# Kernel tuning notes

Hardware: AMD Instinct MI355X
Metric: run time of the kernel (lower is better)

Reference implementation:

```python
import jax, jax.numpy as jnp
import numpy as np

MIN_NEAR = 0.05
DENSITY_SCALE = 1.0
BOUND = 1.0  # spherical scene bounds radius
GEO = 15


def _density_mlp(x, dW1, db1, dW2, db2, dW3, db3):
    h = jax.nn.relu(x @ dW1 + db1)
    h = jax.nn.relu(h @ dW2 + db2)
    h = h @ dW3 + db3  # [M, 1+GEO]
    sigma = jnp.exp(jnp.clip(h[..., 0], -15.0, 15.0))  # trunc_exp
    return sigma, h[..., 1:]


def _color_mlp(d, geo, cW1, cb1, cW2, cb2, cW3, cb3):
    h = jnp.concatenate([d, geo], axis=-1)
    h = jax.nn.relu(h @ cW1 + cb1)
    h = jax.nn.relu(h @ cW2 + cb2)
    return jax.nn.sigmoid(h @ cW3 + cb3)


def _comp_weights(deltas, sigmas):
    # alpha compositing: w_i = alpha_i * prod_{j<i}(1 - alpha_j)
    alphas = 1.0 - jnp.exp(-deltas * sigmas)
    trans = jnp.cumprod(
        jnp.concatenate([jnp.ones_like(alphas[:, :1]), 1.0 - alphas + 1e-15], axis=-1),
        axis=-1)[:, :-1]
    return alphas * trans


def _sample_pdf(bins, weights, n_samples):
    # deterministic importance resampling (eval mode); bins [N,T-1], weights [N,T-2]
    weights = weights + 1e-5
    pdf = weights / jnp.sum(weights, axis=-1, keepdims=True)
    cdf = jnp.cumsum(pdf, axis=-1)
    cdf = jnp.concatenate([jnp.zeros_like(cdf[:, :1]), cdf], axis=-1)  # [N, T-1]
    u = jnp.linspace(0.5 / n_samples, 1.0 - 0.5 / n_samples, n_samples)
    u = jnp.broadcast_to(u, (bins.shape[0], n_samples))
    inds = jax.vmap(lambda c, uu: jnp.searchsorted(c, uu, side='right'))(cdf, u)
    below = jnp.clip(inds - 1, 0, cdf.shape[-1] - 1)
    above = jnp.clip(inds, 0, cdf.shape[-1] - 1)
    cdf_g0 = jnp.take_along_axis(cdf, below, axis=-1)
    cdf_g1 = jnp.take_along_axis(cdf, above, axis=-1)
    bmax = bins.shape[-1] - 1
    bins_g0 = jnp.take_along_axis(bins, jnp.clip(below, 0, bmax), axis=-1)
    bins_g1 = jnp.take_along_axis(bins, jnp.clip(above, 0, bmax), axis=-1)
    denom = jnp.where(cdf_g1 - cdf_g0 < 1e-5, 1.0, cdf_g1 - cdf_g0)
    t = (u - cdf_g0) / denom
    return bins_g0 + t * (bins_g1 - bins_g0)


def _run(rays_o, rays_d, dW1, db1, dW2, db2, dW3, db3,
         cW1, cb1, cW2, cb2, cW3, cb3, num_steps, upsample_steps):
    N = rays_o.shape[0]
    # get_z_val_bounds: ray/sphere intersection, sphere radius BOUND at origin
    b = jnp.sum(rays_o * rays_d, axis=-1)
    c = jnp.sum(rays_o * rays_o, axis=-1) - BOUND ** 2
    disc = jnp.maximum(b * b - c, 0.0)
    z_max = jnp.maximum(-b + jnp.sqrt(disc), MIN_NEAR + 1e-3)
    z_min = jnp.full_like(z_max, MIN_NEAR)
    # get_foreground_z_vals: per-ray linspace (perturb=False)
    t = jnp.linspace(0.0, 1.0, num_steps)
    z_vals = z_min[:, None] + (z_max - z_min)[:, None] * t[None, :]
    z_vals = jnp.clip(z_vals, z_min[:, None], z_max[:, None])
    xyzs = rays_o[:, None, :] + rays_d[:, None, :] * z_vals[..., None]
    sigma, geo = _density_mlp(xyzs.reshape(-1, 3), dW1, db1, dW2, db2, dW3, db3)
    sigma = sigma.reshape(N, num_steps)
    geo = geo.reshape(N, num_steps, GEO)

    # upsample_z_values: importance resampling from coarse weights
    deltas = z_vals[:, 1:] - z_vals[:, :-1]
    aug = jnp.concatenate([deltas, deltas[:, -1:]], axis=-1)
    w_coarse = _comp_weights(aug, DENSITY_SCALE * sigma)
    z_mid = 0.5 * (z_vals[:, :-1] + z_vals[:, 1:])
    new_z = jax.lax.stop_gradient(_sample_pdf(z_mid, w_coarse[:, 1:-1], upsample_steps))
    new_xyzs = rays_o[:, None, :] + rays_d[:, None, :] * new_z[..., None]
    new_sigma, new_geo = _density_mlp(new_xyzs.reshape(-1, 3), dW1, db1, dW2, db2, dW3, db3)
    new_sigma = new_sigma.reshape(N, upsample_steps)
    new_geo = new_geo.reshape(N, upsample_steps, GEO)

    # sort/gather merge of coarse + fine samples
    z_all = jnp.concatenate([z_vals, new_z], axis=1)
    order = jnp.argsort(z_all, axis=1)
    z_vals = jnp.take_along_axis(z_all, order, axis=1)  # [N, T]
    xyzs = jnp.take_along_axis(jnp.concatenate([xyzs, new_xyzs], axis=1), order[..., None], axis=1)
    sigma = jnp.take_along_axis(jnp.concatenate([sigma, new_sigma], axis=1), order, axis=1)
    geo = jnp.take_along_axis(jnp.concatenate([geo, new_geo], axis=1), order[..., None], axis=1)

    deltas = z_vals[:, 1:] - z_vals[:, :-1]
    aug = jnp.concatenate([deltas, deltas[:, -1:]], axis=-1)
    weights = _comp_weights(aug, DENSITY_SCALE * sigma)  # [N, T]

    mask = weights > 1e-4
    dirs = jnp.broadcast_to(rays_d[:, None, :], xyzs.shape).reshape(-1, 3)
    rgb = _color_mlp(dirs, geo.reshape(-1, GEO), cW1, cb1, cW2, cb2, cW3, cb3)
    rgbs = jnp.where(mask.reshape(-1, 1), rgb, 0.0).reshape(N, -1, 3)

    weights_sum = jnp.sum(weights, axis=-1)
    depth = jnp.sum(weights * z_vals, axis=-1)
    image = jnp.sum(weights[..., None] * rgbs, axis=-2)
    bg = 206.0 / 255.0
    image = image + (1.0 - weights_sum)[..., None] * bg

    # pairwise distortion loss (the (z_shifted - z_shifted) term in the source is identically zero)
    sample_dist = 1.0 / num_steps
    z_shift = jnp.concatenate([z_vals[:, 1:], jnp.full((N, 1), sample_dist, z_vals.dtype)], axis=-1)
    mid_zs = 0.5 * z_vals + 0.5 * z_shift
    pair = jnp.abs(mid_zs[:, None, :] - mid_zs[:, :, None]) * (weights[:, None, :] * weights[:, :, None])
    loss = jnp.sum(pair, axis=(1, 2)) / (depth + 1e-6)
    loss = jnp.where(loss < 1e-3, 0.0, loss)  # cutoff
    return jnp.concatenate([image, depth[:, None], loss[:, None]], axis=-1)  # [N, 5]


def setup_inputs() -> dict:
    key = jax.random.key(0)
    ks = jax.random.split(key, 16)
    N, H = 2048, 256
    rays_o = 0.1 * jax.random.normal(ks[0], (N, 3), jnp.float32)  # near scene centre
    rd = jax.random.normal(ks[1], (N, 3), jnp.float32)
    rays_d = rd / jnp.linalg.norm(rd, axis=-1, keepdims=True)

    def w(k, shape):
        return jax.random.normal(k, shape, jnp.float32) * (1.0 / np.sqrt(shape[0]))

    return {
        'rays_o': rays_o, 'rays_d': rays_d,
        'dW1': w(ks[2], (3, H)), 'db1': jnp.zeros(H, jnp.float32),
        'dW2': w(ks[3], (H, H)), 'db2': jnp.zeros(H, jnp.float32),
        'dW3': w(ks[4], (H, 1 + GEO)), 'db3': jnp.zeros(1 + GEO, jnp.float32),
        'cW1': w(ks[5], (3 + GEO, H)), 'cb1': jnp.zeros(H, jnp.float32),
        'cW2': w(ks[6], (H, H)), 'cb2': jnp.zeros(H, jnp.float32),
        'cW3': w(ks[7], (H, 3)), 'cb3': jnp.zeros(3, jnp.float32),
        'num_steps': 128, 'upsample_steps': 128,
    }


def reference(rays_o, rays_d, dW1, db1, dW2, db2, dW3, db3,
              cW1, cb1, cW2, cb2, cW3, cb3, num_steps, upsample_steps):
    return _run(rays_o, rays_d, dW1, db1, dW2, db2, dW3, db3,
                cW1, cb1, cW2, cb2, cW3, cb3, num_steps, upsample_steps)
```

## Files before the change

kernel.cpp:

```cpp
#include <hip/hip_runtime.h>


typedef float f32x4 __attribute__((ext_vector_type(4)));
typedef __bf16 bf16x8 __attribute__((ext_vector_type(8)));
typedef __bf16 bf16x4 __attribute__((ext_vector_type(4)));
typedef unsigned short u16x8 __attribute__((ext_vector_type(8)));
typedef unsigned short u16x4 __attribute__((ext_vector_type(4)));

#define NRAYS 2048
#define NSTEP 128
#define MIN_NEAR 0.05f

#define OFF_D1 0
#define OFF_D2 8192
#define OFF_D3 73728
#define OFF_C1 77824
#define OFF_C2 86016
#define OFF_C3 151552
#define PACK_TOTAL 155648

__device__ __forceinline__ unsigned short f2bf(float f) {
  __bf16 h = (__bf16)f;
  return __builtin_bit_cast(unsigned short, h);
}
__device__ __forceinline__ u16x4 pack4(float a, float b, float c, float d) {
  bf16x4 h;
  h[0] = (__bf16)a; h[1] = (__bf16)b; h[2] = (__bf16)c; h[3] = (__bf16)d;
  return __builtin_bit_cast(u16x4, h);
}

__device__ __forceinline__ float ray_z(const float* __restrict__ ro,
                                       const float* __restrict__ rd, int r, int i) {
  float ox = ro[r * 3], oy = ro[r * 3 + 1], oz = ro[r * 3 + 2];
  float dx = rd[r * 3], dy = rd[r * 3 + 1], dz = rd[r * 3 + 2];
  float b = ox * dx + oy * dy + oz * dz;
  float c = ox * ox + oy * oy + oz * oz - 1.0f;
  float disc = fmaxf(b * b - c, 0.0f);
  float zmax = fmaxf(-b + sqrtf(disc), MIN_NEAR + 1e-3f);
  float zmin = MIN_NEAR;
  float tt = (float)i / 127.0f;
  float zz = zmin + (zmax - zmin) * tt;
  return fminf(fmaxf(zz, zmin), zmax);
}

__device__ __forceinline__ float wave_iscan(float v, int lane) {
#pragma unroll
  for (int off = 1; off < 64; off <<= 1) {
    float y = __shfl_up(v, off, 64);
    if (lane >= off) v += y;
  }
  return v;
}
__device__ __forceinline__ float block_iscan(float v, float* part, int lane, int wid) {
  float s = wave_iscan(v, lane);
  if (lane == 63) part[wid] = s;
  __syncthreads();
  float pre = 0.f;
  if (wid > 0) pre += part[0];
  if (wid > 1) pre += part[1];
  if (wid > 2) pre += part[2];
  return s + pre;
}

__device__ __forceinline__ void pack_std(const float* __restrict__ W,
                                         unsigned short* __restrict__ dst,
                                         int idx, int K, int Norig, int NT) {
  int per = NT * 512;
  int kt = idx / per, rm = idx % per;
  int nt = rm >> 9, lane = (rm >> 3) & 63, j = rm & 7;
  int k = kt * 32 + ((lane >> 4) << 3) + j;
  int n = nt * 16 + (lane & 15);
  float v = (k < K && n < Norig) ? W[k * Norig + n] : 0.0f;
  dst[idx] = f2bf(v);
}

__global__ void k_pack_all(const float* __restrict__ dW1, const float* __restrict__ dW2,
                           const float* __restrict__ dW3, const float* __restrict__ cW1,
                           const float* __restrict__ cW2, const float* __restrict__ cW3,
                           unsigned short* __restrict__ Wp) {
  int idx = blockIdx.x * 256 + threadIdx.x;
  if (idx < OFF_D2) {
    pack_std(dW1, Wp + OFF_D1, idx - OFF_D1, 3, 256, 16);
  } else if (idx < OFF_D3) {
    pack_std(dW2, Wp + OFF_D2, idx - OFF_D2, 256, 256, 16);
  } else if (idx < OFF_C1) {
    int j2 = idx - OFF_D3;
    int lane = (j2 >> 3) & 63, jj = j2 & 7, kt = j2 >> 9;
    int k = kt * 32 + ((lane >> 4) << 3) + jj;
    int n = lane & 15;
    Wp[idx] = f2bf(dW3[k * 16 + ((n + 1) & 15)]);
  } else if (idx < OFF_C2) {
    int j2 = idx - OFF_C1;
    int nt = j2 >> 9, lane = (j2 >> 3) & 63, jj = j2 & 7;
    int k = ((lane >> 4) << 3) + jj;
    int n = nt * 16 + (lane & 15);
    float v = 0.0f;
    if (k < 15) v = cW1[(3 + k) * 256 + n];
    else if (k >= 16 && k < 19) v = cW1[(k - 16) * 256 + n];
    Wp[idx] = f2bf(v);
  } else if (idx < OFF_C3) {
    pack_std(cW2, Wp + OFF_C2, idx - OFF_C2, 256, 256, 16);
  } else if (idx < PACK_TOTAL) {
    pack_std(cW3, Wp + OFF_C3, idx - OFF_C3, 256, 3, 1);
  }
}


__device__ __forceinline__ void mlp_l1(const unsigned short* xb, unsigned short* buf,
                                       const bf16x8 (&w1r)[4], const float* sb1,
                                       int wid, int quad, int col) {
#pragma unroll
  for (int h = 0; h < 2; ++h) {
    f32x4 acc[8];
#pragma unroll
    for (int i = 0; i < 8; ++i) acc[i] = (f32x4){0.f, 0.f, 0.f, 0.f};
    int p0 = (h * 2) * 16 + col, p1 = (h * 2 + 1) * 16 + col;
    bf16x8 x0 = *reinterpret_cast<const bf16x8*>(&xb[p0 * 32 + ((quad ^ (p0 & 3)) * 8)]);
    bf16x8 x1 = *reinterpret_cast<const bf16x8*>(&xb[p1 * 32 + ((quad ^ (p1 & 3)) * 8)]);
#pragma unroll
    for (int ntl = 0; ntl < 4; ++ntl) {
      acc[ntl * 2 + 0] = __builtin_amdgcn_mfma_f32_16x16x32_bf16(w1r[ntl], x0, acc[ntl * 2 + 0], 0, 0, 0);
      acc[ntl * 2 + 1] = __builtin_amdgcn_mfma_f32_16x16x32_bf16(w1r[ntl], x1, acc[ntl * 2 + 1], 0, 0, 0);
    }
#pragma unroll
    for (int ntl = 0; ntl < 4; ++ntl) {
      int n = (wid * 4 + ntl) * 16 + quad * 4;
      f32x4 bv = *reinterpret_cast<const f32x4*>(&sb1[n]);
#pragma unroll
      for (int j = 0; j < 2; ++j) {
        int p = (h * 2 + j) * 16 + col;
        *reinterpret_cast<u16x4*>(&buf[p * 256 + (((n >> 3) ^ (p & 31)) * 8) + (n & 7)]) =
            pack4(fmaxf(acc[ntl * 2 + j][0] + bv[0], 0.f), fmaxf(acc[ntl * 2 + j][1] + bv[1], 0.f),
                  fmaxf(acc[ntl * 2 + j][2] + bv[2], 0.f), fmaxf(acc[ntl * 2 + j][3] + bv[3], 0.f));
      }
    }
  }
}

__device__ __forceinline__ void l2_half_compute(const unsigned short* buf,
                                                const bf16x8 (&w2r)[8][4],
                                                f32x4 (&acc)[8], int h, int quad, int col) {
#pragma unroll
  for (int i = 0; i < 8; ++i) acc[i] = (f32x4){0.f, 0.f, 0.f, 0.f};
#pragma unroll
  for (int kt = 0; kt < 8; ++kt) {
    int p0 = (h * 2) * 16 + col, p1 = (h * 2 + 1) * 16 + col;
    bf16x8 x0 = *reinterpret_cast<const bf16x8*>(&buf[p0 * 256 + (((kt * 4 + quad) ^ (p0 & 31)) * 8)]);
    bf16x8 x1 = *reinterpret_cast<const bf16x8*>(&buf[p1 * 256 + (((kt * 4 + quad) ^ (p1 & 31)) * 8)]);
#pragma unroll
    for (int ntl = 0; ntl < 4; ++ntl) {
      acc[ntl * 2 + 0] = __builtin_amdgcn_mfma_f32_16x16x32_bf16(w2r[kt][ntl], x0, acc[ntl * 2 + 0], 0, 0, 0);
      acc[ntl * 2 + 1] = __builtin_amdgcn_mfma_f32_16x16x32_bf16(w2r[kt][ntl], x1, acc[ntl * 2 + 1], 0, 0, 0);
    }
  }
}

__device__ __forceinline__ void l2_half_write(unsigned short* buf, const f32x4 (&acc)[8],
                                              const float* sb2, int h, int wid, int quad, int col) {
#pragma unroll
  for (int ntl = 0; ntl < 4; ++ntl) {
    int n = (wid * 4 + ntl) * 16 + quad * 4;
    f32x4 bv = *reinterpret_cast<const f32x4*>(&sb2[n]);
#pragma unroll
    for (int j = 0; j < 2; ++j) {
      int p = (h * 2 + j) * 16 + col;
      *reinterpret_cast<u16x4*>(&buf[p * 256 + (((n >> 3) ^ (p & 31)) * 8) + (n & 7)]) =
          pack4(fmaxf(acc[ntl * 2 + j][0] + bv[0], 0.f), fmaxf(acc[ntl * 2 + j][1] + bv[1], 0.f),
                fmaxf(acc[ntl * 2 + j][2] + bv[2], 0.f), fmaxf(acc[ntl * 2 + j][3] + bv[3], 0.f));
    }
  }
}

template <bool FIRST>
__global__ __launch_bounds__(256, 2)
void k_density(const float* __restrict__ ro, const float* __restrict__ rd,
               const float* __restrict__ zin,
               const unsigned short* __restrict__ Wp1, const float* __restrict__ b1,
               const unsigned short* __restrict__ Wp2, const float* __restrict__ b2,
               const unsigned short* __restrict__ Wp3, const float* __restrict__ b3,
               unsigned short* __restrict__ gout, float* __restrict__ sig,
               float* __restrict__ z_f) {
  __shared__ __align__(16) unsigned short buf[64 * 256];
  __shared__ __align__(16) unsigned short xb[64 * 32];
  __shared__ __align__(16) unsigned short sW3[4096];
  __shared__ __align__(16) float sb1[256];
  __shared__ __align__(16) float sb2[256];
  __shared__ __align__(16) float sb3[16];
  __shared__ __align__(16) float ssig[256];
  __shared__ __align__(16) float sred[16];
  const int t = threadIdx.x;
  const int lane = t & 63, wid = t >> 6, quad = lane >> 4, col = lane & 15;
  const int p_ = t >> 2, g_ = t & 3;

  sb1[t] = b1[t];
  sb2[t] = b2[t];
  if (t < 16) sb3[t] = b3[(t + 1) & 15];
  { const u16x8* s = (const u16x8*)Wp3; u16x8* d = (u16x8*)sW3;
    d[t] = s[t]; d[t + 256] = s[t + 256]; }

  bf16x8 w1r[4], w2r[8][4];
#pragma unroll
  for (int ntl = 0; ntl < 4; ++ntl)
    w1r[ntl] = *reinterpret_cast<const bf16x8*>(Wp1 + ((wid * 4 + ntl) * 64 + lane) * 8);
#pragma unroll
  for (int kt = 0; kt < 8; ++kt)
#pragma unroll
    for (int ntl = 0; ntl < 4; ++ntl)
      w2r[kt][ntl] = *reinterpret_cast<const bf16x8*>(Wp2 + ((kt * 16 + wid * 4 + ntl) * 64 + lane) * 8);

#pragma unroll 1
  for (int tt = 0; tt < 4; ++tt) {
    const int P0 = blockIdx.x * 256 + tt * 64;
    {
      u16x8 pk = {0, 0, 0, 0, 0, 0, 0, 0};
      if (g_ == 0) {
        int P = P0 + p_;
        int rr_ = P >> 7, ii = P & 127;
        float zz;
        if constexpr (FIRST) zz = ray_z(ro, rd, rr_, ii);
        else zz = zin[P];
        pk[0] = f2bf(ro[rr_ * 3 + 0] + rd[rr_ * 3 + 0] * zz);
        pk[1] = f2bf(ro[rr_ * 3 + 1] + rd[rr_ * 3 + 1] * zz);
        pk[2] = f2bf(ro[rr_ * 3 + 2] + rd[rr_ * 3 + 2] * zz);
      }
      *reinterpret_cast<u16x8*>(&xb[p_ * 32 + ((g_ ^ (p_ & 3)) * 8)]) = pk;
    }
    __syncthreads();
    mlp_l1(xb, buf, w1r, sb1, wid, quad, col);
    __syncthreads();
    f32x4 acc[8];
    l2_half_compute(buf, w2r, acc, 0, quad, col);
    __syncthreads();
    l2_half_write(buf, acc, sb2, 0, wid, quad, col);
    l2_half_compute(buf, w2r, acc, 1, quad, col);
    __syncthreads();
    l2_half_write(buf, acc, sb2, 1, wid, quad, col);
    __syncthreads();
    {
      const int p = wid * 16 + col;
      f32x4 a3 = {0.f, 0.f, 0.f, 0.f};
#pragma unroll
      for (int kt = 0; kt < 8; ++kt) {
        bf16x8 w = *reinterpret_cast<const bf16x8*>(&sW3[(kt * 64 + lane) * 8]);
        bf16x8 xx = *reinterpret_cast<const bf16x8*>(&buf[p * 256 + (((kt * 4 + quad) ^ (p & 31)) * 8)]);
        a3 = __builtin_amdgcn_mfma_f32_16x16x32_bf16(w, xx, a3, 0, 0, 0);
      }
      int n0 = quad * 4;
      float v0 = a3[0] + sb3[n0], v1 = a3[1] + sb3[n0 + 1];
      float v2 = a3[2] + sb3[n0 + 2], v3 = a3[3] + sb3[n0 + 3];
      if (quad == 3) {
        float sgm = __expf(fminf(fmaxf(v3, -15.f), 15.f));
        sig[P0 + p] = sgm;
        if constexpr (FIRST) ssig[tt * 64 + p] = sgm;
        v3 = 0.0f;
      }
      *reinterpret_cast<u16x4*>(gout + (size_t)(P0 + p) * 16 + n0) = pack4(v0, v1, v2, v3);
    }
  }

  if constexpr (FIRST) {
    __syncthreads();
    float* psz = reinterpret_cast<float*>(buf);
    float* pmid = psz + 256;
    float* pcdf = psz + 512;
    float* psw = psz + 768;
    const int segw = t >> 7;
    const int i = t & 127;
    const int seg = segw * 128;
    const int rg = blockIdx.x * 2 + segw;
    float zi = ray_z(ro, rd, rg, i);
    psz[seg + i] = zi;
    float sgv = ssig[t];
    __syncthreads();
    float aug = (i < 127) ? psz[seg + i + 1] - zi : psz[seg + 127] - psz[seg + 126];
    float alpha = 1.0f - __expf(-aug * sgv);
    float lt = __logf(1.0f - alpha + 1e-15f);
    float s = wave_iscan(lt, lane);
    if (lane == 63) sred[wid] = s;
    __syncthreads();
    if (wid & 1) s += sred[wid - 1];
    float w = alpha * __expf(s - lt);
    psw[seg + i] = w;
    if (i < 127) pmid[seg + i] = 0.5f * (zi + psz[seg + i + 1]);
    __syncthreads();
    float v2s = (i < 126) ? psw[seg + i + 1] + 1e-5f : 0.f;
    float s2 = wave_iscan(v2s, lane);
    if (lane == 63) sred[8 + wid] = s2;
    __syncthreads();
    if (wid & 1) s2 += sred[8 + wid - 1];
    psw[seg + i] = s2;
    __syncthreads();
    float total = psw[seg + 125];
    if (i <= 126) pcdf[seg + i] = (i == 0) ? 0.f : psw[seg + i - 1] / total;
    __syncthreads();
    const float lo = 0.5f / 128.0f, hi = 1.0f - 0.5f / 128.0f;
    float u = lo + (hi - lo) * ((float)i / 127.0f);
    int loI = 0, hiI = 127;
    while (loI < hiI) {
      int mid = (loI + hiI) >> 1;
      if (pcdf[seg + mid] > u) hiI = mid; else loI = mid + 1;
    }
    int below = loI - 1; if (below < 0) below = 0; if (below > 126) below = 126;
    int above = loI;     if (above > 126) above = 126;
    float c0 = pcdf[seg + below], c1 = pcdf[seg + above];
    float b0v = pmid[seg + below], b1v = pmid[seg + above];
    float dn = c1 - c0; if (dn < 1e-5f) dn = 1.0f;
    float ttt = (u - c0) / dn;
    z_f[rg * NSTEP + i] = b0v + ttt * (b1v - b0v);
  }
}

__global__ __launch_bounds__(256, 2)
void k_mcf(const float* __restrict__ ro, const float* __restrict__ rd,
           const float* __restrict__ z_f,
           const float* __restrict__ sigc, const float* __restrict__ sigf,
           const unsigned short* __restrict__ goutc, const unsigned short* __restrict__ goutf,
           const unsigned short* __restrict__ Wp1, const float* __restrict__ cb1,
           const unsigned short* __restrict__ Wp2, const float* __restrict__ cb2,
           const unsigned short* __restrict__ Wp3, const float* __restrict__ cb3,
           float* __restrict__ out) {
  __shared__ __align__(16) unsigned short buf[64 * 256];
  __shared__ __align__(16) unsigned short xb[64 * 32];
  __shared__ __align__(16) unsigned short sW3[4096];
  __shared__ __align__(16) float sb1[256];
  __shared__ __align__(16) float sb2[256];
  __shared__ __align__(16) float szm[256];
  __shared__ __align__(16) float swgt[256];
  __shared__ __align__(16) float srgb[768];
  __shared__ __align__(16) float sred[48];
  __shared__ unsigned short sord[256];
  const int t = threadIdx.x;
  const int lane = t & 63, wid = t >> 6, quad = lane >> 4, col = lane & 15;
  const int p_ = t >> 2, g_ = t & 3;
  const int r = blockIdx.x;

  sb1[t] = cb1[t];
  sb2[t] = cb2[t];
  { const u16x8* s = (const u16x8*)Wp3; u16x8* d = (u16x8*)sW3;
    d[t] = s[t]; d[t + 256] = s[t + 256]; }

  bf16x8 w1r[4], w2r[8][4];
#pragma unroll
  for (int ntl = 0; ntl < 4; ++ntl)
    w1r[ntl] = *reinterpret_cast<const bf16x8*>(Wp1 + ((wid * 4 + ntl) * 64 + lane) * 8);
#pragma unroll
  for (int kt = 0; kt < 8; ++kt)
#pragma unroll
    for (int ntl = 0; ntl < 4; ++ntl)
      w2r[kt][ntl] = *reinterpret_cast<const bf16x8*>(Wp2 + ((kt * 16 + wid * 4 + ntl) * 64 + lane) * 8);

  float* szc = reinterpret_cast<float*>(buf);
  float* szf = szc + 128;
  if (t < 128) szc[t] = ray_z(ro, rd, r, t);
  else szf[t - 128] = z_f[r * NSTEP + (t - 128)];
  __syncthreads();
  int pos; float myz;
  if (t < 128) {
    myz = szc[t];
    int lo = 0, hi = 128;
    while (lo < hi) { int m = (lo + hi) >> 1; if (szf[m] < myz) lo = m + 1; else hi = m; }
    pos = t + lo;
  } else {
    int j = t - 128; myz = szf[j];
    int lo = 0, hi = 128;
    while (lo < hi) { int m = (lo + hi) >> 1; if (szc[m] <= myz) lo = m + 1; else hi = m; }
    pos = j + lo;
  }
  szm[pos] = myz; sord[pos] = (unsigned short)t;
  __syncthreads();
  int srci = sord[t];
  float sg = (srci < 128) ? sigc[r * NSTEP + srci] : sigf[r * NSTEP + (srci - 128)];
  float zt = szm[t];
  float aug = (t < 255) ? szm[t + 1] - zt : szm[255] - szm[254];
  float alpha = 1.0f - __expf(-aug * sg);
  float lt = __logf(1.0f - alpha + 1e-15f);
  float incl = block_iscan(lt, sred, lane, wid);
  swgt[t] = alpha * __expf(incl - lt);
  __syncthreads();

  float dv0 = rd[r * 3], dv1 = rd[r * 3 + 1], dv2 = rd[r * 3 + 2];
  u16x8 dirpk = {f2bf(dv0), f2bf(dv1), f2bf(dv2), 0, 0, 0, 0, 0};
  u16x8 gx = {0, 0, 0, 0, 0, 0, 0, 0};
  float wgtv = 0.0f;
  {
    if (g_ < 2) {
      int s0 = sord[p_];
      const unsigned short* gs = ((s0 < 128) ? goutc : goutf)
          + ((size_t)(r * NSTEP + (s0 & 127)) * 16) + g_ * 8;
      gx = *reinterpret_cast<const u16x8*>(gs);
    } else if (g_ == 2) {
      gx = dirpk;
    } else {
      wgtv = swgt[p_];
    }
  }
#pragma unroll 1
  for (int tt = 0; tt < 4; ++tt) {
    const int haveNext = (tt < 3);
    int go = __syncthreads_or((g_ == 3) && (wgtv > 1e-4f));
    int ordn = 0; float wgtn = 0.0f;
    u16x8 gxn = {0, 0, 0, 0, 0, 0, 0, 0};
    if (go) {
      *reinterpret_cast<u16x8*>(&xb[p_ * 32 + ((g_ ^ (p_ & 3)) * 8)]) = gx;
      __syncthreads();
      mlp_l1(xb, buf, w1r, sb1, wid, quad, col);
      __syncthreads();
    }
    if (haveNext) {
      int Pn = (tt + 1) * 64 + p_;
      if (g_ < 2) ordn = sord[Pn];
      else if (g_ == 2) gxn = dirpk;
      else wgtn = swgt[Pn];
    }
    f32x4 acc[8];
    if (go) {
      l2_half_compute(buf, w2r, acc, 0, quad, col);
      __syncthreads();
      l2_half_write(buf, acc, sb2, 0, wid, quad, col);
    }
    if (haveNext && g_ < 2) {
      const unsigned short* gs = ((ordn < 128) ? goutc : goutf)
          + ((size_t)(r * NSTEP + (ordn & 127)) * 16) + g_ * 8;
      gxn = *reinterpret_cast<const u16x8*>(gs);
    }
    if (go) {
      l2_half_compute(buf, w2r, acc, 1, quad, col);
      __syncthreads();
      l2_half_write(buf, acc, sb2, 1, wid, quad, col);
      __syncthreads();
      {
        const int p = wid * 16 + col;
        f32x4 a3 = {0.f, 0.f, 0.f, 0.f};
#pragma unroll
        for (int kt = 0; kt < 8; ++kt) {
          bf16x8 w = *reinterpret_cast<const bf16x8*>(&sW3[(kt * 64 + lane) * 8]);
          bf16x8 xx = *reinterpret_cast<const bf16x8*>(&buf[p * 256 + (((kt * 4 + quad) ^ (p & 31)) * 8)]);
          a3 = __builtin_amdgcn_mfma_f32_16x16x32_bf16(w, xx, a3, 0, 0, 0);
        }
        if (quad == 0) {
          int pi = tt * 64 + p;
          srgb[pi * 3 + 0] = 1.0f / (1.0f + __expf(-(a3[0] + cb3[0])));
          srgb[pi * 3 + 1] = 1.0f / (1.0f + __expf(-(a3[1] + cb3[1])));
          srgb[pi * 3 + 2] = 1.0f / (1.0f + __expf(-(a3[2] + cb3[2])));
        }
      }
    }
    gx = gxn; wgtv = wgtn;
  }

  __syncthreads();
  float ztf = szm[t], wtf = swgt[t];
  float znext = (t < 255) ? szm[t + 1] : (1.0f / 128.0f);
  float mt = 0.5f * ztf + 0.5f * znext;
  float cr = 0.f, cg = 0.f, cbl = 0.f;
  if (wtf > 1e-4f) { cr = srgb[t * 3]; cg = srgb[t * 3 + 1]; cbl = srgb[t * 3 + 2]; }
  if (t == 255) { sred[36] = mt; sred[37] = wtf; }
  float wm = (t < 255) ? wtf : 0.f;
  float Pw = block_iscan(wm, sred, lane, wid);
  float Ps = block_iscan(wm * mt, sred + 4, lane, wid);
  float W254 = sred[0] + sred[1] + sred[2] + sred[3];
  float S254 = sred[4] + sred[5] + sred[6] + sred[7];
  float m255 = sred[36], w255 = sred[37];
  float contrib = 0.f;
  if (t < 255)
    contrib = wtf * (mt * (2.f * Pw - W254) - (2.f * Ps - S254))
            + 2.f * wtf * fabsf(mt - m255) * w255;
  float vals[6] = {wtf, wtf * ztf, wtf * cr, wtf * cg, wtf * cbl, contrib};
#pragma unroll
  for (int k = 0; k < 6; ++k) {
    float v = vals[k];
#pragma unroll
    for (int m = 1; m < 64; m <<= 1) v += __shfl_xor(v, m, 64);
    if (lane == 0) sred[8 + k * 4 + wid] = v;
  }
  __syncthreads();
  if (t == 0) {
    float a6[6];
#pragma unroll
    for (int k = 0; k < 6; ++k)
      a6[k] = sred[8 + k * 4] + sred[8 + k * 4 + 1] + sred[8 + k * 4 + 2] + sred[8 + k * 4 + 3];
    const float bgc = 206.0f / 255.0f;
    float wsum = a6[0], depth = a6[1];
    float loss = a6[5] / (depth + 1e-6f);
    if (loss < 1e-3f) loss = 0.0f;
    out[r * 5 + 0] = a6[2] + (1.0f - wsum) * bgc;
    out[r * 5 + 1] = a6[3] + (1.0f - wsum) * bgc;
    out[r * 5 + 2] = a6[4] + (1.0f - wsum) * bgc;
    out[r * 5 + 3] = depth;
    out[r * 5 + 4] = loss;
  }
}

extern "C" void kernel_launch(void* const* d_in, const int* in_sizes, int n_in,
                              void* d_out, int out_size, void* d_ws, size_t ws_size,
                              hipStream_t stream) {
  const float* rays_o = (const float*)d_in[0];
  const float* rays_d = (const float*)d_in[1];
  const float* dW1 = (const float*)d_in[2];
  const float* db1 = (const float*)d_in[3];
  const float* dW2 = (const float*)d_in[4];
  const float* db2 = (const float*)d_in[5];
  const float* dW3 = (const float*)d_in[6];
  const float* db3 = (const float*)d_in[7];
  const float* cW1 = (const float*)d_in[8];
  const float* cb1 = (const float*)d_in[9];
  const float* cW2 = (const float*)d_in[10];
  const float* cb2 = (const float*)d_in[11];
  const float* cW3 = (const float*)d_in[12];
  const float* cb3 = (const float*)d_in[13];

  char* ws = (char*)d_ws;
  size_t off = 0;
  auto alloc = [&](size_t bytes) -> void* {
    void* p = ws + off;
    off += (bytes + 255) & ~(size_t)255;
    return p;
  };
  unsigned short* Wp = (unsigned short*)alloc((size_t)PACK_TOTAL * 2);
  unsigned short* goutc = (unsigned short*)alloc((size_t)NRAYS * NSTEP * 16 * 2);
  unsigned short* goutf = (unsigned short*)alloc((size_t)NRAYS * NSTEP * 16 * 2);
  float* sigc = (float*)alloc((size_t)NRAYS * NSTEP * 4);
  float* sigf = (float*)alloc((size_t)NRAYS * NSTEP * 4);
  float* z_f  = (float*)alloc((size_t)NRAYS * NSTEP * 4);
  (void)ws_size; (void)in_sizes; (void)n_in; (void)out_size;

  k_pack_all<<<PACK_TOTAL / 256, 256, 0, stream>>>(dW1, dW2, dW3, cW1, cW2, cW3, Wp);

  k_density<true><<<(NRAYS * NSTEP) / 256, 256, 0, stream>>>(
      rays_o, rays_d, nullptr,
      Wp + OFF_D1, db1, Wp + OFF_D2, db2, Wp + OFF_D3, db3, goutc, sigc, z_f);
  k_density<false><<<(NRAYS * NSTEP) / 256, 256, 0, stream>>>(
      rays_o, rays_d, z_f,
      Wp + OFF_D1, db1, Wp + OFF_D2, db2, Wp + OFF_D3, db3, goutf, sigf, nullptr);
  k_mcf<<<NRAYS, 256, 0, stream>>>(
      rays_o, rays_d, z_f, sigc, sigf, goutc, goutf,
      Wp + OFF_C1, cb1, Wp + OFF_C2, cb2, Wp + OFF_C3, cb3, (float*)d_out);
}
```

Before: 272.2 us.

## Cut register pressure to fit three blocks per CU in MLP kernels

Restructures the layer-2 MFMA loop to process one 16-point quarter at a time (4 accumulators instead of 8), reloads layer-1 weights from global inside mlp_l1 instead of keeping them resident, and drops the software prefetch of the next tile's gathered features in the color kernel. The aim is to lower VGPR usage enough to raise launch bounds from 2 to 3 blocks per CU, improving latency hiding. The cost is more block barriers per tile (four instead of two in layer 2), repeated layer-1 weight loads, and the loss of load/compute overlap from the removed prefetch.

```diff
diff --git a/kernel.cpp b/kernel.cpp
--- a/kernel.cpp
+++ b/kernel.cpp
@@ -106,73 +106,57 @@
 }
 
 
-__device__ __forceinline__ void mlp_l1(const unsigned short* xb, unsigned short* buf,
-                                       const bf16x8 (&w1r)[4], const float* sb1,
-                                       int wid, int quad, int col) {
-#pragma unroll
-  for (int h = 0; h < 2; ++h) {
-    f32x4 acc[8];
-#pragma unroll
-    for (int i = 0; i < 8; ++i) acc[i] = (f32x4){0.f, 0.f, 0.f, 0.f};
-    int p0 = (h * 2) * 16 + col, p1 = (h * 2 + 1) * 16 + col;
-    bf16x8 x0 = *reinterpret_cast<const bf16x8*>(&xb[p0 * 32 + ((quad ^ (p0 & 3)) * 8)]);
-    bf16x8 x1 = *reinterpret_cast<const bf16x8*>(&xb[p1 * 32 + ((quad ^ (p1 & 3)) * 8)]);
-#pragma unroll
-    for (int ntl = 0; ntl < 4; ++ntl) {
-      acc[ntl * 2 + 0] = __builtin_amdgcn_mfma_f32_16x16x32_bf16(w1r[ntl], x0, acc[ntl * 2 + 0], 0, 0, 0);
-      acc[ntl * 2 + 1] = __builtin_amdgcn_mfma_f32_16x16x32_bf16(w1r[ntl], x1, acc[ntl * 2 + 1], 0, 0, 0);
-    }
-#pragma unroll
-    for (int ntl = 0; ntl < 4; ++ntl) {
-      int n = (wid * 4 + ntl) * 16 + quad * 4;
-      f32x4 bv = *reinterpret_cast<const f32x4*>(&sb1[n]);
-#pragma unroll
-      for (int j = 0; j < 2; ++j) {
-        int p = (h * 2 + j) * 16 + col;
-        *reinterpret_cast<u16x4*>(&buf[p * 256 + (((n >> 3) ^ (p & 31)) * 8) + (n & 7)]) =
-            pack4(fmaxf(acc[ntl * 2 + j][0] + bv[0], 0.f), fmaxf(acc[ntl * 2 + j][1] + bv[1], 0.f),
-                  fmaxf(acc[ntl * 2 + j][2] + bv[2], 0.f), fmaxf(acc[ntl * 2 + j][3] + bv[3], 0.f));
-      }
-    }
-  }
-}
-
-__device__ __forceinline__ void l2_half_compute(const unsigned short* buf,
-                                                const bf16x8 (&w2r)[8][4],
-                                                f32x4 (&acc)[8], int h, int quad, int col) {
-#pragma unroll
-  for (int i = 0; i < 8; ++i) acc[i] = (f32x4){0.f, 0.f, 0.f, 0.f};
-#pragma unroll
-  for (int kt = 0; kt < 8; ++kt) {
-    int p0 = (h * 2) * 16 + col, p1 = (h * 2 + 1) * 16 + col;
-    bf16x8 x0 = *reinterpret_cast<const bf16x8*>(&buf[p0 * 256 + (((kt * 4 + quad) ^ (p0 & 31)) * 8)]);
-    bf16x8 x1 = *reinterpret_cast<const bf16x8*>(&buf[p1 * 256 + (((kt * 4 + quad) ^ (p1 & 31)) * 8)]);
-#pragma unroll
-    for (int ntl = 0; ntl < 4; ++ntl) {
-      acc[ntl * 2 + 0] = __builtin_amdgcn_mfma_f32_16x16x32_bf16(w2r[kt][ntl], x0, acc[ntl * 2 + 0], 0, 0, 0);
-      acc[ntl * 2 + 1] = __builtin_amdgcn_mfma_f32_16x16x32_bf16(w2r[kt][ntl], x1, acc[ntl * 2 + 1], 0, 0, 0);
-    }
-  }
-}
-
-__device__ __forceinline__ void l2_half_write(unsigned short* buf, const f32x4 (&acc)[8],
-                                              const float* sb2, int h, int wid, int quad, int col) {
+__device__ __forceinline__ void epi_store(unsigned short* buf, const f32x4 (&acc)[4],
+                                          const float* bias, int p, int wid, int quad) {
 #pragma unroll
   for (int ntl = 0; ntl < 4; ++ntl) {
     int n = (wid * 4 + ntl) * 16 + quad * 4;
-    f32x4 bv = *reinterpret_cast<const f32x4*>(&sb2[n]);
-#pragma unroll
-    for (int j = 0; j < 2; ++j) {
-      int p = (h * 2 + j) * 16 + col;
-      *reinterpret_cast<u16x4*>(&buf[p * 256 + (((n >> 3) ^ (p & 31)) * 8) + (n & 7)]) =
-          pack4(fmaxf(acc[ntl * 2 + j][0] + bv[0], 0.f), fmaxf(acc[ntl * 2 + j][1] + bv[1], 0.f),
-                fmaxf(acc[ntl * 2 + j][2] + bv[2], 0.f), fmaxf(acc[ntl * 2 + j][3] + bv[3], 0.f));
-    }
+    f32x4 bv = *reinterpret_cast<const f32x4*>(&bias[n]);
+    *reinterpret_cast<u16x4*>(&buf[p * 256 + (((n >> 3) ^ (p & 31)) * 8) + (n & 7)]) =
+        pack4(fmaxf(acc[ntl][0] + bv[0], 0.f), fmaxf(acc[ntl][1] + bv[1], 0.f),
+              fmaxf(acc[ntl][2] + bv[2], 0.f), fmaxf(acc[ntl][3] + bv[3], 0.f));
+  }
+}
+
+__device__ __forceinline__ void mlp_l1(const unsigned short* xb, unsigned short* buf,
+                                       const unsigned short* __restrict__ Wp1,
+                                       const float* sb1,
+                                       int wid, int quad, int col, int lane) {
+  bf16x8 w1r[4];
+#pragma unroll
+  for (int ntl = 0; ntl < 4; ++ntl)
+    w1r[ntl] = *reinterpret_cast<const bf16x8*>(Wp1 + ((wid * 4 + ntl) * 64 + lane) * 8);
+#pragma unroll
+  for (int pt = 0; pt < 4; ++pt) {
+    const int p = pt * 16 + col;
+    bf16x8 x = *reinterpret_cast<const bf16x8*>(&xb[p * 32 + ((quad ^ (p & 3)) * 8)]);
+    f32x4 acc[4];
+#pragma unroll
+    for (int i = 0; i < 4; ++i) acc[i] = (f32x4){0.f, 0.f, 0.f, 0.f};
+#pragma unroll
+    for (int ntl = 0; ntl < 4; ++ntl)
+      acc[ntl] = __builtin_amdgcn_mfma_f32_16x16x32_bf16(w1r[ntl], x, acc[ntl], 0, 0, 0);
+    epi_store(buf, acc, sb1, p, wid, quad);
+  }
+}
+
+__device__ __forceinline__ void l2_q_compute(const unsigned short* buf,
+                                             const bf16x8 (&w2r)[8][4],
+                                             f32x4 (&acc)[4], int q, int quad, int col) {
+#pragma unroll
+  for (int i = 0; i < 4; ++i) acc[i] = (f32x4){0.f, 0.f, 0.f, 0.f};
+  const int p = q * 16 + col;
+#pragma unroll
+  for (int kt = 0; kt < 8; ++kt) {
+    bf16x8 x = *reinterpret_cast<const bf16x8*>(&buf[p * 256 + (((kt * 4 + quad) ^ (p & 31)) * 8)]);
+#pragma unroll
+    for (int ntl = 0; ntl < 4; ++ntl)
+      acc[ntl] = __builtin_amdgcn_mfma_f32_16x16x32_bf16(w2r[kt][ntl], x, acc[ntl], 0, 0, 0);
   }
 }
 
 template <bool FIRST>
-__global__ __launch_bounds__(256, 2)
+__global__ __launch_bounds__(256, 3)
 void k_density(const float* __restrict__ ro, const float* __restrict__ rd,
                const float* __restrict__ zin,
                const unsigned short* __restrict__ Wp1, const float* __restrict__ b1,
@@ -198,10 +182,7 @@
   { const u16x8* s = (const u16x8*)Wp3; u16x8* d = (u16x8*)sW3;
     d[t] = s[t]; d[t + 256] = s[t + 256]; }
 
-  bf16x8 w1r[4], w2r[8][4];
-#pragma unroll
-  for (int ntl = 0; ntl < 4; ++ntl)
-    w1r[ntl] = *reinterpret_cast<const bf16x8*>(Wp1 + ((wid * 4 + ntl) * 64 + lane) * 8);
+  bf16x8 w2r[8][4];
 #pragma unroll
   for (int kt = 0; kt < 8; ++kt)
 #pragma unroll
@@ -226,15 +207,15 @@
       *reinterpret_cast<u16x8*>(&xb[p_ * 32 + ((g_ ^ (p_ & 3)) * 8)]) = pk;
     }
     __syncthreads();
-    mlp_l1(xb, buf, w1r, sb1, wid, quad, col);
-    __syncthreads();
-    f32x4 acc[8];
-    l2_half_compute(buf, w2r, acc, 0, quad, col);
-    __syncthreads();
-    l2_half_write(buf, acc, sb2, 0, wid, quad, col);
-    l2_half_compute(buf, w2r, acc, 1, quad, col);
-    __syncthreads();
-    l2_half_write(buf, acc, sb2, 1, wid, quad, col);
+    mlp_l1(xb, buf, Wp1, sb1, wid, quad, col, lane);
+    __syncthreads();
+#pragma unroll 1
+    for (int q = 0; q < 4; ++q) {
+      f32x4 acc[4];
+      l2_q_compute(buf, w2r, acc, q, quad, col);
+      __syncthreads();
+      epi_store(buf, acc, sb2, q * 16 + col, wid, quad);
+    }
     __syncthreads();
     {
       const int p = wid * 16 + col;
@@ -310,7 +291,7 @@
   }
 }
 
-__global__ __launch_bounds__(256, 2)
+__global__ __launch_bounds__(256, 3)
 void k_mcf(const float* __restrict__ ro, const float* __restrict__ rd,
            const float* __restrict__ z_f,
            const float* __restrict__ sigc, const float* __restrict__ sigf,
@@ -339,10 +320,7 @@
   { const u16x8* s = (const u16x8*)Wp3; u16x8* d = (u16x8*)sW3;
     d[t] = s[t]; d[t + 256] = s[t + 256]; }
 
-  bf16x8 w1r[4], w2r[8][4];
-#pragma unroll
-  for (int ntl = 0; ntl < 4; ++ntl)
-    w1r[ntl] = *reinterpret_cast<const bf16x8*>(Wp1 + ((wid * 4 + ntl) * 64 + lane) * 8);
+  bf16x8 w2r[8][4];
 #pragma unroll
   for (int kt = 0; kt < 8; ++kt)
 #pragma unroll
@@ -379,54 +357,33 @@
   __syncthreads();
 
   float dv0 = rd[r * 3], dv1 = rd[r * 3 + 1], dv2 = rd[r * 3 + 2];
-  u16x8 dirpk = {f2bf(dv0), f2bf(dv1), f2bf(dv2), 0, 0, 0, 0, 0};
-  u16x8 gx = {0, 0, 0, 0, 0, 0, 0, 0};
-  float wgtv = 0.0f;
-  {
-    if (g_ < 2) {
-      int s0 = sord[p_];
-      const unsigned short* gs = ((s0 < 128) ? goutc : goutf)
-          + ((size_t)(r * NSTEP + (s0 & 127)) * 16) + g_ * 8;
-      gx = *reinterpret_cast<const u16x8*>(gs);
-    } else if (g_ == 2) {
-      gx = dirpk;
-    } else {
-      wgtv = swgt[p_];
-    }
-  }
 #pragma unroll 1
   for (int tt = 0; tt < 4; ++tt) {
-    const int haveNext = (tt < 3);
-    int go = __syncthreads_or((g_ == 3) && (wgtv > 1e-4f));
-    int ordn = 0; float wgtn = 0.0f;
-    u16x8 gxn = {0, 0, 0, 0, 0, 0, 0, 0};
+    int pred = (t < 64) && (swgt[tt * 64 + t] > 1e-4f);
+    int go = __syncthreads_or(pred);
     if (go) {
-      *reinterpret_cast<u16x8*>(&xb[p_ * 32 + ((g_ ^ (p_ & 3)) * 8)]) = gx;
+      {
+        u16x8 pk = {0, 0, 0, 0, 0, 0, 0, 0};
+        if (g_ < 2) {
+          int s0 = sord[tt * 64 + p_];
+          const unsigned short* gs = ((s0 < 128) ? goutc : goutf)
+              + ((size_t)(r * NSTEP + (s0 & 127)) * 16) + g_ * 8;
+          pk = *reinterpret_cast<const u16x8*>(gs);
+        } else if (g_ == 2) {
+          pk[0] = f2bf(dv0); pk[1] = f2bf(dv1); pk[2] = f2bf(dv2);
+        }
+        *reinterpret_cast<u16x8*>(&xb[p_ * 32 + ((g_ ^ (p_ & 3)) * 8)]) = pk;
+      }
       __syncthreads();
-      mlp_l1(xb, buf, w1r, sb1, wid, quad, col);
+      mlp_l1(xb, buf, Wp1, sb1, wid, quad, col, lane);
       __syncthreads();
-    }
-    if (haveNext) {
-      int Pn = (tt + 1) * 64 + p_;
-      if (g_ < 2) ordn = sord[Pn];
-      else if (g_ == 2) gxn = dirpk;
-      else wgtn = swgt[Pn];
-    }
-    f32x4 acc[8];
-    if (go) {
-      l2_half_compute(buf, w2r, acc, 0, quad, col);
-      __syncthreads();
-      l2_half_write(buf, acc, sb2, 0, wid, quad, col);
-    }
-    if (haveNext && g_ < 2) {
-      const unsigned short* gs = ((ordn < 128) ? goutc : goutf)
-          + ((size_t)(r * NSTEP + (ordn & 127)) * 16) + g_ * 8;
-      gxn = *reinterpret_cast<const u16x8*>(gs);
-    }
-    if (go) {
-      l2_half_compute(buf, w2r, acc, 1, quad, col);
-      __syncthreads();
-      l2_half_write(buf, acc, sb2, 1, wid, quad, col);
+#pragma unroll 1
+      for (int q = 0; q < 4; ++q) {
+        f32x4 acc[4];
+        l2_q_compute(buf, w2r, acc, q, quad, col);
+        __syncthreads();
+        epi_store(buf, acc, sb2, q * 16 + col, wid, quad);
+      }
       __syncthreads();
       {
         const int p = wid * 16 + col;
@@ -445,7 +402,6 @@
         }
       }
     }
-    gx = gxn; wgtv = wgtn;
   }
 
   __syncthreads();
```

Result: slower. 574.6 us (+111.1%).
